# Performance work log

Measured on AMD Instinct MI355X. Metric: run time of the kernel, lower is better.

Reference implementation:

```python
import jax, jax.numpy as jnp
import numpy as np

N, D, K = 32768, 256, 2048
BETA = 0.25  # init arg beta, in [0,1) branch of the loss


def setup_inputs() -> dict:
    key = jax.random.key(0)
    k1, k2 = jax.random.split(key)
    x = jax.random.normal(k1, (N, D), dtype=jnp.float32)
    # mimics nn.Embedding init: uniform(-1/K, 1/K) then mean-centered
    cb = jax.random.uniform(k2, (K, D), dtype=jnp.float32, minval=-1.0 / K, maxval=1.0 / K)
    codebook = cb - cb.mean(axis=0)
    return {"x": x, "codebook": codebook}


def reference(x, codebook):
    # pairwise squared L2 distances: [N, K]
    dist = (
        jnp.sum(x * x, axis=1, keepdims=True)
        + jnp.sum(codebook * codebook, axis=1)
        - 2.0 * jnp.matmul(x, codebook.T)
    )
    encoding_inds = jnp.argmin(dist, axis=1)  # [N]
    # one-hot @ codebook == gather of nearest code vectors
    x_codebook = jnp.take(codebook, encoding_inds, axis=0)  # [N, D]
    # straight-through quantization
    x_quantized = x + jax.lax.stop_gradient(x_codebook - x)
    # VQ loss, beta in [0, 1) branch
    commit = jnp.mean((x - jax.lax.stop_gradient(x_codebook)) ** 2)
    embed = jnp.mean((x_codebook - jax.lax.stop_gradient(x)) ** 2)
    loss = BETA * commit + embed
    return x_quantized, loss
```

## Files before the change

### kernel.cpp

```cpp
#include <hip/hip_runtime.h>

#define N_ROWS 32768
#define DIM    256
#define KCODES 2048
#define CSCALE 4096.0f
#define BROWS  32

typedef __attribute__((ext_vector_type(16))) float f32x16;
typedef __attribute__((ext_vector_type(4)))  unsigned int u32x4;

union frag16 { u32x4 v; long l[2]; };

#define SWAIT(s) asm volatile("s_waitcnt " s)

__device__ __forceinline__ void gl16(const void* g, void* l) {
    __builtin_amdgcn_global_load_lds(
        (const __attribute__((address_space(1))) unsigned int*)g,
        (__attribute__((address_space(3))) unsigned int*)l, 16, 0, 0);
}

__device__ __forceinline__ u32x4 ldsr128(const void* p) {
    const unsigned a =
        (unsigned)(unsigned long long)(__attribute__((address_space(3))) const char*)p;
    u32x4 d;
    asm volatile("ds_read_b128 %0, %1" : "=&v"(d) : "v"(a));
    return d;
}

__device__ __forceinline__ uint4 pack16(const float* s) {
    int a = __builtin_amdgcn_cvt_pk_fp8_f32(s[0],  s[1],  0, false);
    a     = __builtin_amdgcn_cvt_pk_fp8_f32(s[2],  s[3],  a, true);
    int b = __builtin_amdgcn_cvt_pk_fp8_f32(s[4],  s[5],  0, false);
    b     = __builtin_amdgcn_cvt_pk_fp8_f32(s[6],  s[7],  b, true);
    int c = __builtin_amdgcn_cvt_pk_fp8_f32(s[8],  s[9],  0, false);
    c     = __builtin_amdgcn_cvt_pk_fp8_f32(s[10], s[11], c, true);
    int d = __builtin_amdgcn_cvt_pk_fp8_f32(s[12], s[13], 0, false);
    d     = __builtin_amdgcn_cvt_pk_fp8_f32(s[14], s[15], d, true);
    uint4 o; o.x = a; o.y = b; o.z = c; o.w = d;
    return o;
}


__global__ void prep_cb(const float* __restrict__ cb, unsigned int* __restrict__ cbf8,
                        float* __restrict__ halfcn, float* __restrict__ loss) {
    const int t    = threadIdx.x;
    const int code = blockIdx.x * 4 + (t >> 6);
    const int s    = t & 63;
    if (blockIdx.x == 0 && t == 0) *loss = 0.0f;
    const int kc = s >> 4, d = (s >> 2) & 3, b4 = (s & 3) * 4;
    const int h = d >> 1, q = d & 1;
    const int k0 = kc * 64 + q * 32 + (b4 >> 3) * 16 + h * 8 + (b4 & 7);
    float4 v = *(const float4*)&cb[(size_t)code * DIM + k0];
    int pk = __builtin_amdgcn_cvt_pk_fp8_f32(v.x * CSCALE, v.y * CSCALE, 0, false);
    pk     = __builtin_amdgcn_cvt_pk_fp8_f32(v.z * CSCALE, v.w * CSCALE, pk, true);
    cbf8[(size_t)code * 64 + s] = (unsigned int)pk;
    float ssum = v.x * v.x + v.y * v.y + v.z * v.z + v.w * v.w;
    #pragma unroll
    for (int o = 32; o > 0; o >>= 1) ssum += __shfl_down(ssum, o, 64);
    if (s == 0) halfcn[code] = 0.5f * CSCALE * ssum;
}

__global__ __launch_bounds__(256, 3) void vq_fused(
        const float* __restrict__ x, const float* __restrict__ cb,
        const char* __restrict__ cbf8, const float* __restrict__ halfcn,
        float* __restrict__ out, float* __restrict__ loss) {
    __shared__ char As[4][2048];
    __shared__ char Bs[2][4][4096];
    struct Tail { float red[BROWS][4]; int idxs[BROWS]; float lred[4]; };
    Tail* tl = (Tail*)As;

    const int t    = threadIdx.x;
    const int lane = t & 63;
    const int w    = t >> 6;
    const int l32  = lane & 31;
    const int h    = lane >> 5;
    const int row0 = blockIdx.x * BROWS;

    {
        const int r   = t >> 3;
        const int kc  = (t >> 1) & 3;
        const int pp  = t & 1;
        const int key = (r >> 1) & 3;
        const float* src = x + (size_t)(row0 + r) * DIM + kc * 64;
        float buf[16];
        #pragma unroll
        for (int pi = 0; pi < 2; pi++) {
            const int p = pp * 2 + pi;
            const int d = p ^ key, hh = d >> 1, qq = d & 1;
            #pragma unroll
            for (int j = 0; j < 4; j++) *(float4*)(buf + j * 4) =
                *(const float4*)(src + qq * 32 + (j >> 1) * 16 + hh * 8 + (j & 1) * 4);
            *(uint4*)(As[kc] + r * 64 + p * 16) = pack16(buf);
        }
    }

    float hcv[8][2];
    #pragma unroll
    for (int p = 0; p < 8; p++) {
        hcv[p][0] = halfcn[p * 256 + w * 64 + l32];
        hcv[p][1] = halfcn[p * 256 + w * 64 + 32 + l32];
    }

    const int lsub = lane >> 2;
    const int lpos = lane & 3;
    auto stageB = [&](int j) {
        const int pass_ = j >> 2, kc_ = j & 3;
        char* dst = Bs[j & 1][w];
        #pragma unroll
        for (int r_ = 0; r_ < 4; r_++) {
            const int lc = r_ * 16 + lsub;
            const int g  = lpos ^ ((lc >> 1) & 3);
            const char* src = cbf8 + (size_t)(pass_ * 256 + w * 64 + lc) * 256
                              + kc_ * 64 + g * 16;
            gl16(src, dst + r_ * 1024);
        }
    };

    const int key = (l32 >> 1) & 3;
    const int p0  = (h * 2 + 0) ^ key;
    const int p1  = (h * 2 + 1) ^ key;

    frag16 af[2][2];
    frag16 bf[2][2][2];

    float mp[16];
    #pragma unroll
    for (int r = 0; r < 16; r++) mp[r] = -3.0e38f;

    __syncthreads();

    {
        const char* ab = As[0];
        const int rbase = l32 * 64;
        af[0][0].v = ldsr128(ab + rbase + p0 * 16);
        af[0][1].v = ldsr128(ab + rbase + p1 * 16);
    }
    stageB(0); stageB(1);
    SWAIT("vmcnt(4)");
    {
        const char* bb = Bs[0][w];
        #pragma unroll
        for (int ct = 0; ct < 2; ct++) {
            const int cbase = (ct * 32 + l32) * 64;
            bf[0][ct][0].v = ldsr128(bb + cbase + p0 * 16);
            bf[0][ct][1].v = ldsr128(bb + cbase + p1 * 16);
        }
    }

    #pragma unroll
    for (int pass = 0; pass < 8; ++pass) {
        f32x16 acc[2];
        #pragma unroll
        for (int r = 0; r < 16; r++) {
            acc[0][r] = -hcv[pass][0];
            acc[1][r] = -hcv[pass][1];
        }

        #pragma unroll
        for (int kc = 0; kc < 4; ++kc) {
            const int i  = pass * 4 + kc;
            const int cs = kc & 1;
            const int ns = cs ^ 1;

            SWAIT("lgkmcnt(0)");
            __builtin_amdgcn_sched_barrier(0);

            if (i + 2 < 32) {
                stageB(i + 2);
                SWAIT("vmcnt(4)");
            } else if (i == 30) {
                SWAIT("vmcnt(0)");
            }

            if (i + 1 < 32) {
                const char* ab = As[(kc + 1) & 3];
                const char* bb = Bs[(i + 1) & 1][w];
                const int rbase = l32 * 64;
                af[ns][0].v = ldsr128(ab + rbase + p0 * 16);
                af[ns][1].v = ldsr128(ab + rbase + p1 * 16);
                #pragma unroll
                for (int ct = 0; ct < 2; ct++) {
                    const int cbase = (ct * 32 + l32) * 64;
                    bf[ns][ct][0].v = ldsr128(bb + cbase + p0 * 16);
                    bf[ns][ct][1].v = ldsr128(bb + cbase + p1 * 16);
                }
            }

            __builtin_amdgcn_s_setprio(1);
            #pragma unroll
            for (int q = 0; q < 2; q++)
                #pragma unroll
                for (int hf = 0; hf < 2; hf++)
                    #pragma unroll
                    for (int ct = 0; ct < 2; ct++)
                        acc[ct] = __builtin_amdgcn_mfma_f32_32x32x16_fp8_fp8(
                            af[cs][q].l[hf], bf[cs][ct][q].l[hf],
                            acc[ct], 0, 0, 0);
            __builtin_amdgcn_s_setprio(0);
        }

        #pragma unroll
        for (int ct = 0; ct < 2; ct++) {
            const unsigned code = (unsigned)(pass * 256 + w * 64 + ct * 32 + l32);
            #pragma unroll
            for (int r = 0; r < 16; r++) {
                unsigned u = (__float_as_uint(acc[ct][r]) & 0xFFFFF800u) | code;
                mp[r] = fmaxf(mp[r], __uint_as_float(u));
            }
        }
    }

    #pragma unroll
    for (int m = 1; m <= 16; m <<= 1)
        #pragma unroll
        for (int r = 0; r < 16; r++)
            mp[r] = fmaxf(mp[r], __shfl_xor(mp[r], m, 64));

    __syncthreads();

    if (l32 == 0) {
        #pragma unroll
        for (int r = 0; r < 16; r++) {
            const int row = (r & 3) + 8 * (r >> 2) + 4 * h;
            tl->red[row][w] = mp[r];
        }
    }
    __syncthreads();
    if (t < BROWS) {
        float b0 = fmaxf(fmaxf(tl->red[t][0], tl->red[t][1]),
                         fmaxf(tl->red[t][2], tl->red[t][3]));
        tl->idxs[t] = (int)(__float_as_uint(b0) & 2047u);
    }
    __syncthreads();

    float lsum = 0.0f;
    #pragma unroll 4
    for (int r = 0; r < BROWS; r++) {
        const int code = tl->idxs[r];
        const float c  = cb[(size_t)code * DIM + t];
        const float xv = x[(size_t)(row0 + r) * DIM + t];
        out[(size_t)(row0 + r) * DIM + t] = c;
        const float d = xv - c;
        lsum += d * d;
    }
    #pragma unroll
    for (int o = 32; o > 0; o >>= 1) lsum += __shfl_down(lsum, o, 64);
    if (lane == 0) tl->lred[w] = lsum;
    __syncthreads();
    if (t == 0) {
        const float scale = 1.25f / (float)((size_t)N_ROWS * DIM);
        atomicAdd(loss, (tl->lred[0] + tl->lred[1] + tl->lred[2] + tl->lred[3]) * scale);
    }
}

extern "C" void kernel_launch(void* const* d_in, const int* in_sizes, int n_in,
                              void* d_out, int out_size, void* d_ws, size_t ws_size,
                              hipStream_t stream) {
    const float* x  = (const float*)d_in[0];
    const float* cb = (const float*)d_in[1];
    float* out  = (float*)d_out;
    float* loss = out + (size_t)N_ROWS * DIM;

    char* ws = (char*)d_ws;
    unsigned int* cbf8 = (unsigned int*)ws;
    float* halfcn = (float*)(ws + (size_t)KCODES * 256);

    prep_cb<<<KCODES / 4, 256, 0, stream>>>(cb, cbf8, halfcn, loss);
    vq_fused<<<N_ROWS / BROWS, 256, 0, stream>>>(x, cb, (const char*)cbf8, halfcn, out, loss);
}
```

Before: 130.4 us.

## Pre-layout codebook as MFMA fragments and load B directly into registers

A new prep kernel writes the FP8 codebook already arranged in per-lane MFMA fragment order. The main kernel then loads B operands straight from global memory into registers, using a three-deep register prefetch ring, instead of staging them through LDS with async global-to-LDS copies and waitcnt handling. The half-norms are cached in LDS, and all four A k-chunks are held in registers up front. This drops the B LDS buffers and the LDS read traffic, at the cost of more VGPR pressure, relying on L2 for codebook reuse across blocks, and one extra kernel launch.

```diff
diff --git a/kernel.cpp b/kernel.cpp
--- a/kernel.cpp
+++ b/kernel.cpp
@@ -10,22 +10,6 @@
 typedef __attribute__((ext_vector_type(4)))  unsigned int u32x4;
 
 union frag16 { u32x4 v; long l[2]; };
-
-#define SWAIT(s) asm volatile("s_waitcnt " s)
-
-__device__ __forceinline__ void gl16(const void* g, void* l) {
-    __builtin_amdgcn_global_load_lds(
-        (const __attribute__((address_space(1))) unsigned int*)g,
-        (__attribute__((address_space(3))) unsigned int*)l, 16, 0, 0);
-}
-
-__device__ __forceinline__ u32x4 ldsr128(const void* p) {
-    const unsigned a =
-        (unsigned)(unsigned long long)(__attribute__((address_space(3))) const char*)p;
-    u32x4 d;
-    asm volatile("ds_read_b128 %0, %1" : "=&v"(d) : "v"(a));
-    return d;
-}
 
 __device__ __forceinline__ uint4 pack16(const float* s) {
     int a = __builtin_amdgcn_cvt_pk_fp8_f32(s[0],  s[1],  0, false);
@@ -40,9 +24,8 @@
     return o;
 }
 
-
-__global__ void prep_cb(const float* __restrict__ cb, unsigned int* __restrict__ cbf8,
-                        float* __restrict__ halfcn, float* __restrict__ loss) {
+__global__ void prep_h(const float* __restrict__ cb,
+                       float* __restrict__ halfcn, float* __restrict__ loss) {
     const int t    = threadIdx.x;
     const int code = blockIdx.x * 4 + (t >> 6);
     const int s    = t & 63;
@@ -51,21 +34,40 @@
     const int h = d >> 1, q = d & 1;
     const int k0 = kc * 64 + q * 32 + (b4 >> 3) * 16 + h * 8 + (b4 & 7);
     float4 v = *(const float4*)&cb[(size_t)code * DIM + k0];
-    int pk = __builtin_amdgcn_cvt_pk_fp8_f32(v.x * CSCALE, v.y * CSCALE, 0, false);
-    pk     = __builtin_amdgcn_cvt_pk_fp8_f32(v.z * CSCALE, v.w * CSCALE, pk, true);
-    cbf8[(size_t)code * 64 + s] = (unsigned int)pk;
     float ssum = v.x * v.x + v.y * v.y + v.z * v.z + v.w * v.w;
     #pragma unroll
     for (int o = 32; o > 0; o >>= 1) ssum += __shfl_down(ssum, o, 64);
     if (s == 0) halfcn[code] = 0.5f * CSCALE * ssum;
 }
 
+__global__ void prep_frag(const float* __restrict__ cb, uint4* __restrict__ cbF) {
+    const int gid = blockIdx.x * 256 + threadIdx.x;
+    const int L   = gid & 63;
+    const int r   = gid >> 6;
+    const int j   = r & 1;
+    const int ct  = (r >> 1) & 1;
+    const int w   = (r >> 2) & 3;
+    const int i   = r >> 4;
+    const int pass = i >> 2, kc = i & 3;
+    const int h   = L >> 5, l32 = L & 31;
+    const int code = pass * 256 + w * 64 + ct * 32 + l32;
+    float buf[16];
+    #pragma unroll
+    for (int b = 0; b < 4; b++) {
+        const int k0 = kc * 64 + j * 32 + (b >> 1) * 16 + h * 8 + (b & 1) * 4;
+        float4 v = *(const float4*)&cb[(size_t)code * DIM + k0];
+        buf[b * 4 + 0] = v.x * CSCALE; buf[b * 4 + 1] = v.y * CSCALE;
+        buf[b * 4 + 2] = v.z * CSCALE; buf[b * 4 + 3] = v.w * CSCALE;
+    }
+    cbF[gid] = pack16(buf);
+}
+
 __global__ __launch_bounds__(256, 3) void vq_fused(
         const float* __restrict__ x, const float* __restrict__ cb,
-        const char* __restrict__ cbf8, const float* __restrict__ halfcn,
+        const uint4* __restrict__ cbF, const float* __restrict__ halfcn,
         float* __restrict__ out, float* __restrict__ loss) {
     __shared__ char As[4][2048];
-    __shared__ char Bs[2][4][4096];
+    __shared__ float hcs[KCODES];
     struct Tail { float red[BROWS][4]; int idxs[BROWS]; float lred[4]; };
     Tail* tl = (Tail*)As;
 
@@ -92,101 +94,64 @@
                 *(const float4*)(src + qq * 32 + (j >> 1) * 16 + hh * 8 + (j & 1) * 4);
             *(uint4*)(As[kc] + r * 64 + p * 16) = pack16(buf);
         }
-    }
-
-    float hcv[8][2];
-    #pragma unroll
-    for (int p = 0; p < 8; p++) {
-        hcv[p][0] = halfcn[p * 256 + w * 64 + l32];
-        hcv[p][1] = halfcn[p * 256 + w * 64 + 32 + l32];
-    }
-
-    const int lsub = lane >> 2;
-    const int lpos = lane & 3;
-    auto stageB = [&](int j) {
-        const int pass_ = j >> 2, kc_ = j & 3;
-        char* dst = Bs[j & 1][w];
-        #pragma unroll
-        for (int r_ = 0; r_ < 4; r_++) {
-            const int lc = r_ * 16 + lsub;
-            const int g  = lpos ^ ((lc >> 1) & 3);
-            const char* src = cbf8 + (size_t)(pass_ * 256 + w * 64 + lc) * 256
-                              + kc_ * 64 + g * 16;
-            gl16(src, dst + r_ * 1024);
-        }
-    };
+        #pragma unroll
+        for (int jj = 0; jj < 8; jj++) hcs[jj * 256 + t] = halfcn[jj * 256 + t];
+    }
 
     const int key = (l32 >> 1) & 3;
     const int p0  = (h * 2 + 0) ^ key;
     const int p1  = (h * 2 + 1) ^ key;
 
-    frag16 af[2][2];
-    frag16 bf[2][2][2];
-
     float mp[16];
     #pragma unroll
     for (int r = 0; r < 16; r++) mp[r] = -3.0e38f;
 
-    __syncthreads();
-
-    {
-        const char* ab = As[0];
+    const char* bbase = (const char*)cbF + w * 4096 + (size_t)lane * 16;
+
+    frag16 bfr[3][4];
+    #pragma unroll
+    for (int s = 0; s < 3; s++)
+        #pragma unroll
+        for (int c = 0; c < 4; c++)
+            bfr[s][c].v = *(const u32x4*)(bbase + s * 16384 + c * 1024);
+
+    __syncthreads();
+
+    frag16 afr[4][2];
+    #pragma unroll
+    for (int kc = 0; kc < 4; kc++) {
+        const char* ab = As[kc];
         const int rbase = l32 * 64;
-        af[0][0].v = ldsr128(ab + rbase + p0 * 16);
-        af[0][1].v = ldsr128(ab + rbase + p1 * 16);
-    }
-    stageB(0); stageB(1);
-    SWAIT("vmcnt(4)");
-    {
-        const char* bb = Bs[0][w];
-        #pragma unroll
-        for (int ct = 0; ct < 2; ct++) {
-            const int cbase = (ct * 32 + l32) * 64;
-            bf[0][ct][0].v = ldsr128(bb + cbase + p0 * 16);
-            bf[0][ct][1].v = ldsr128(bb + cbase + p1 * 16);
-        }
+        afr[kc][0].v = *(const u32x4*)(ab + rbase + p0 * 16);
+        afr[kc][1].v = *(const u32x4*)(ab + rbase + p1 * 16);
     }
 
     #pragma unroll
     for (int pass = 0; pass < 8; ++pass) {
+        const float hc0 = hcs[pass * 256 + w * 64 + l32];
+        const float hc1 = hcs[pass * 256 + w * 64 + 32 + l32];
         f32x16 acc[2];
         #pragma unroll
         for (int r = 0; r < 16; r++) {
-            acc[0][r] = -hcv[pass][0];
-            acc[1][r] = -hcv[pass][1];
+            acc[0][r] = -hc0;
+            acc[1][r] = -hc1;
         }
 
         #pragma unroll
         for (int kc = 0; kc < 4; ++kc) {
             const int i  = pass * 4 + kc;
-            const int cs = kc & 1;
-            const int ns = cs ^ 1;
-
-            SWAIT("lgkmcnt(0)");
-            __builtin_amdgcn_sched_barrier(0);
-
-            if (i + 2 < 32) {
-                stageB(i + 2);
-                SWAIT("vmcnt(4)");
-            } else if (i == 30) {
-                SWAIT("vmcnt(0)");
+            const int sl = i % 3;
+
+            frag16 cur[4];
+            #pragma unroll
+            for (int c = 0; c < 4; c++) cur[c] = bfr[sl][c];
+
+            if (i + 3 < 32) {
+                #pragma unroll
+                for (int c = 0; c < 4; c++)
+                    bfr[sl][c].v = *(const u32x4*)(bbase + (i + 3) * 16384 + c * 1024);
             }
 
-            if (i + 1 < 32) {
-                const char* ab = As[(kc + 1) & 3];
-                const char* bb = Bs[(i + 1) & 1][w];
-                const int rbase = l32 * 64;
-                af[ns][0].v = ldsr128(ab + rbase + p0 * 16);
-                af[ns][1].v = ldsr128(ab + rbase + p1 * 16);
-                #pragma unroll
-                for (int ct = 0; ct < 2; ct++) {
-                    const int cbase = (ct * 32 + l32) * 64;
-                    bf[ns][ct][0].v = ldsr128(bb + cbase + p0 * 16);
-                    bf[ns][ct][1].v = ldsr128(bb + cbase + p1 * 16);
-                }
-            }
-
-            __builtin_amdgcn_s_setprio(1);
             #pragma unroll
             for (int q = 0; q < 2; q++)
                 #pragma unroll
@@ -194,9 +159,8 @@
                     #pragma unroll
                     for (int ct = 0; ct < 2; ct++)
                         acc[ct] = __builtin_amdgcn_mfma_f32_32x32x16_fp8_fp8(
-                            af[cs][q].l[hf], bf[cs][ct][q].l[hf],
+                            afr[kc][q].l[hf], cur[ct * 2 + q].l[hf],
                             acc[ct], 0, 0, 0);
-            __builtin_amdgcn_s_setprio(0);
         }
 
         #pragma unroll
@@ -262,9 +226,10 @@
     float* loss = out + (size_t)N_ROWS * DIM;
 
     char* ws = (char*)d_ws;
-    unsigned int* cbf8 = (unsigned int*)ws;
+    uint4* cbF    = (uint4*)ws;
     float* halfcn = (float*)(ws + (size_t)KCODES * 256);
 
-    prep_cb<<<KCODES / 4, 256, 0, stream>>>(cb, cbf8, halfcn, loss);
-    vq_fused<<<N_ROWS / BROWS, 256, 0, stream>>>(x, cb, (const char*)cbf8, halfcn, out, loss);
-}
+    prep_h   <<<KCODES / 4, 256, 0, stream>>>(cb, halfcn, loss);
+    prep_frag<<<128,        256, 0, stream>>>(cb, cbF);
+    vq_fused <<<N_ROWS / BROWS, 256, 0, stream>>>(x, cb, cbF, halfcn, out, loss);
+}
```

Result: faster. 123.2 us (-5.5%).
